# Kernel optimization log

Hardware: AMD Instinct MI355X
Metric: run time of the kernel (lower is better)

The kernel has to match this reference:

```python
import jax, jax.numpy as jnp
import numpy as np

N_NODES = 100000
N_EDGES = 1600000
D_IN = 128
D_OUT = 128


def setup_inputs() -> dict:
    key = jax.random.key(0)
    k1, k2, k3, k4, k5 = jax.random.split(key, 5)
    h = jax.random.normal(k1, (N_NODES, D_IN), dtype=jnp.float32)
    src = jax.random.randint(k2, (N_EDGES,), 0, N_NODES, dtype=jnp.int64)
    dst = jax.random.randint(k3, (N_EDGES,), 0, N_NODES, dtype=jnp.int64)
    # Glorot-ish init for linear weights (PyTorch nn.Linear style: [out, in])
    scale = 1.0 / np.sqrt(D_IN)
    W_self = jax.random.uniform(k4, (D_OUT, D_IN), jnp.float32, -scale, scale)
    W_neigh = jax.random.uniform(k5, (D_OUT, D_IN), jnp.float32, -scale, scale)
    b = jnp.zeros((D_OUT,), dtype=jnp.float32)
    return {"h": h, "src": src, "dst": dst, "W_self": W_self,
            "W_neigh": W_neigh, "b": b}


def reference(h, src, dst, W_self, W_neigh, b):
    n_nodes = h.shape[0]
    # neighbor gather + segment-mean over in-neighbors (DGL fn.copy_u + fn.mean)
    msg = h[src]                                            # [E, D_in]
    neigh_sum = jax.ops.segment_sum(msg, dst, num_segments=n_nodes)
    deg = jax.ops.segment_sum(jnp.ones_like(dst, dtype=h.dtype), dst,
                              num_segments=n_nodes)         # [N]
    h_neigh = neigh_sum / jnp.maximum(deg, 1.0)[:, None]    # mean; 0 for isolated
    # SAGEConv mean: fc_self(h) + fc_neigh(h_neigh) + bias
    out = h @ W_self.T + h_neigh @ W_neigh.T + b
    return out
```

## Files before the change

kernel.cpp:

```cpp
#include <hip/hip_runtime.h>
#include <stdint.h>

#define NN 100000
#define NE 1600000
#define DD 128
#define NTILES ((NN + 127) / 128)
#define NB 512
#define CHUNK (NE / NB)
#define NBUCK ((NN + 255) / 256)
#define BCAP 4608
#define QCAP 1536

typedef __bf16 bf16x8 __attribute__((ext_vector_type(8)));
typedef float f32x4 __attribute__((ext_vector_type(4)));
typedef float f32x2 __attribute__((ext_vector_type(2)));

__device__ __forceinline__ unsigned int f2bf2(float a, float b) {
  union { float f; unsigned u; } x, y;
  x.f = a; y.f = b;
  unsigned ua = x.u + (0x7FFFu + ((x.u >> 16) & 1u));
  unsigned ub = y.u + (0x7FFFu + ((y.u >> 16) & 1u));
  return (ua >> 16) | (ub & 0xFFFF0000u);
}

__global__ __launch_bounds__(256) void zero_kernel(int* __restrict__ gcur) {
  int t = blockIdx.x * 256 + threadIdx.x;
  if (t < NBUCK) gcur[t] = 0;
}

__global__ __launch_bounds__(256) void convert_scatter_kernel(
    const float4* __restrict__ hp, uint2* __restrict__ h8,
    uint4* __restrict__ hbf, const int* __restrict__ src,
    const int* __restrict__ dst, int* __restrict__ gcur,
    unsigned* __restrict__ ebuf) {
  __shared__ int lhp[512];
  __shared__ int lbase[NBUCK];
  __shared__ int lcur[NBUCK];
  __shared__ int gstart[NBUCK];
  __shared__ unsigned sdata[CHUNK];
  __shared__ int sgpos[CHUNK];
  int t = threadIdx.x, b = blockIdx.x;
  int gid = b * 256 + t;
  float4 a = hp[2 * gid], c = hp[2 * gid + 1];
  int lo = __builtin_amdgcn_cvt_pk_fp8_f32(a.x, a.y, 0, false);
  lo = __builtin_amdgcn_cvt_pk_fp8_f32(a.z, a.w, lo, true);
  int hi = __builtin_amdgcn_cvt_pk_fp8_f32(c.x, c.y, 0, false);
  hi = __builtin_amdgcn_cvt_pk_fp8_f32(c.z, c.w, hi, true);
  h8[gid] = make_uint2((unsigned)lo, (unsigned)hi);

  uint4 q;
  q.x = f2bf2(a.x, a.y);
  q.y = f2bf2(a.z, a.w);
  q.z = f2bf2(c.x, c.y);
  q.w = f2bf2(c.z, c.w);
  int m = t >> 4, c8 = t & 15;
  int rt = b & 7, kc = c8 >> 2, quad = c8 & 3;
  hbf[(size_t)(b >> 3) * 2048 + (((rt << 2) + kc) << 6) + (quad << 4) + m] = q;

  if (b >= NB) return;

  lhp[t] = 0;
  lhp[t + 256] = 0;
  __syncthreads();
  int e0 = b * CHUNK;
  for (int e = e0 + t; e < e0 + CHUNK; e += 256)
    atomicAdd(&lhp[dst[e] >> 8], 1);
  __syncthreads();
  int c0 = lhp[t], c1 = lhp[t + 256];
  for (int d = 1; d < 512; d <<= 1) {
    int x0 = (t >= d) ? lhp[t - d] : 0;
    int x1 = ((t + 256) >= d) ? lhp[t + 256 - d] : 0;
    __syncthreads();
    lhp[t] += x0;
    lhp[t + 256] += x1;
    __syncthreads();
  }
  if (t < NBUCK) {
    lbase[t] = lhp[t] - c0;
    lcur[t] = 0;
    gstart[t] = t * BCAP + (c0 ? atomicAdd(&gcur[t], c0) : 0);
  }
  int i2 = t + 256;
  if (i2 < NBUCK) {
    lbase[i2] = lhp[i2] - c1;
    lcur[i2] = 0;
    gstart[i2] = i2 * BCAP + (c1 ? atomicAdd(&gcur[i2], c1) : 0);
  }
  __syncthreads();
  for (int e = e0 + t; e < e0 + CHUNK; e += 256) {
    int d = dst[e], s = src[e];
    int bk = d >> 8;
    int slot = atomicAdd(&lcur[bk], 1);
    int lp = lbase[bk] + slot;
    sdata[lp] = ((unsigned)(d & 255) << 24) | (unsigned)s;
    sgpos[lp] = gstart[bk] + slot;
  }
  __syncthreads();
  for (int j = t; j < CHUNK; j += 256) ebuf[sgpos[j]] = sdata[j];
}

__device__ __forceinline__ void acc16p(f32x2* a, uint4 u) {
  a[0] += __builtin_amdgcn_cvt_pk_f32_fp8(u.x, false);
  a[1] += __builtin_amdgcn_cvt_pk_f32_fp8(u.x, true);
  a[2] += __builtin_amdgcn_cvt_pk_f32_fp8(u.y, false);
  a[3] += __builtin_amdgcn_cvt_pk_f32_fp8(u.y, true);
  a[4] += __builtin_amdgcn_cvt_pk_f32_fp8(u.z, false);
  a[5] += __builtin_amdgcn_cvt_pk_f32_fp8(u.z, true);
  a[6] += __builtin_amdgcn_cvt_pk_f32_fp8(u.w, false);
  a[7] += __builtin_amdgcn_cvt_pk_f32_fp8(u.w, true);
}

__global__ __launch_bounds__(256, 8) void gather_bucket_kernel(
    const unsigned* __restrict__ ebuf, const int* __restrict__ gcur,
    const uint4* __restrict__ h8, uint4* __restrict__ hfrag) {
  __shared__ int hist[64], st[64], cur[64];
  __shared__ int ssort[QCAP];
  int t = threadIdx.x, bid = blockIdx.x;
  int g = bid >> 2, qt = bid & 3;
  int base = g * BCAP;
  int cnt = gcur[g];
  int lo = qt * 64;
  if (t < 64) hist[t] = 0;
  __syncthreads();
  for (int j = t; j < cnt; j += 256) {
    int dn = (int)(ebuf[base + j] >> 24) - lo;
    if ((unsigned)dn < 64u) atomicAdd(&hist[dn], 1);
  }
  __syncthreads();
  if (t < 64) st[t] = hist[t];
  __syncthreads();
  for (int d = 1; d < 64; d <<= 1) {
    int x = (t < 64 && t >= d) ? st[t - d] : 0;
    __syncthreads();
    if (t < 64) st[t] += x;
    __syncthreads();
  }
  if (t < 64) {
    int s = st[t] - hist[t];
    st[t] = s;
    cur[t] = s;
  }
  __syncthreads();
  for (int j = t; j < cnt; j += 256) {
    unsigned e = ebuf[base + j];
    int dn = (int)(e >> 24) - lo;
    if ((unsigned)dn < 64u) {
      int pos = atomicAdd(&cur[dn], 1);
      if (pos < QCAP) ssort[pos] = (int)(e & 0x00FFFFFFu);
    }
  }
  __syncthreads();
  int grp = t >> 3, l = t & 7;
  uint4* bp = hfrag + (size_t)(bid >> 1) * 2048;
#pragma unroll 1
  for (int rnd = 0; rnd < 2; rnd++) {
    int li = rnd * 32 + grp;
    int deg = hist[li];
    int j0 = st[li];
    f32x2 a[8];
#pragma unroll
    for (int i = 0; i < 8; i++) a[i] = f32x2{0.f, 0.f};
    int jmax = deg & ~3;
    if (jmax > 0) {
      int s0 = ssort[j0], s1 = ssort[j0 + 1], s2 = ssort[j0 + 2], s3 = ssort[j0 + 3];
      uint4 u0 = h8[(size_t)s0 * 8 + l];
      uint4 u1 = h8[(size_t)s1 * 8 + l];
      uint4 u2 = h8[(size_t)s2 * 8 + l];
      uint4 u3 = h8[(size_t)s3 * 8 + l];
      for (int j4 = 4; j4 < jmax; j4 += 4) {
        int t0 = ssort[j0 + j4], t1 = ssort[j0 + j4 + 1];
        int t2 = ssort[j0 + j4 + 2], t3 = ssort[j0 + j4 + 3];
        uint4 v0 = h8[(size_t)t0 * 8 + l];
        uint4 v1 = h8[(size_t)t1 * 8 + l];
        uint4 v2 = h8[(size_t)t2 * 8 + l];
        uint4 v3 = h8[(size_t)t3 * 8 + l];
        acc16p(a, u0); acc16p(a, u1); acc16p(a, u2); acc16p(a, u3);
        u0 = v0; u1 = v1; u2 = v2; u3 = v3;
      }
      acc16p(a, u0); acc16p(a, u1); acc16p(a, u2); acc16p(a, u3);
    }
    for (int j2 = jmax; j2 < deg; j2++) acc16p(a, h8[(size_t)ssort[j0 + j2] * 8 + l]);
    float sc = (deg > 0) ? (1.0f / (float)deg) : 0.0f;
    f32x2 s2 = {sc, sc};
#pragma unroll
    for (int i = 0; i < 8; i++) a[i] *= s2;
    uint4 r0, r1;
    r0.x = f2bf2(a[0].x, a[0].y);  r0.y = f2bf2(a[1].x, a[1].y);
    r0.z = f2bf2(a[2].x, a[2].y);  r0.w = f2bf2(a[3].x, a[3].y);
    r1.x = f2bf2(a[4].x, a[4].y);  r1.y = f2bf2(a[5].x, a[5].y);
    r1.z = f2bf2(a[6].x, a[6].y);  r1.w = f2bf2(a[7].x, a[7].y);
    int r = ((qt & 1) << 6) + li;
    int rt = r >> 4, m = r & 15;
    int kc = l >> 1, quad = (l & 1) << 1;
    int slot = (((rt << 2) + kc) << 6) + (quad << 4) + m;
    bp[slot] = r0;
    bp[slot + 16] = r1;
  }
}

__device__ __forceinline__ void stage_w(const float* __restrict__ X,
                                        uint4* buf, int t) {
#pragma unroll
  for (int i = 0; i < 8; i++) {
    int id = t + (i << 8);
    int r = id >> 4;
    int c8 = id & 15;
    const float4* p = (const float4*)(X + (size_t)r * DD + (c8 << 3));
    float4 v0 = p[0], v1 = p[1];
    uint4 q;
    q.x = f2bf2(v0.x, v0.y);
    q.y = f2bf2(v0.z, v0.w);
    q.z = f2bf2(v1.x, v1.y);
    q.w = f2bf2(v1.z, v1.w);
    int rt = r >> 4, m = r & 15, kc = c8 >> 2, quad = c8 & 3;
    buf[(((rt << 2) + kc) << 6) + (quad << 4) + m] = q;
  }
}

__device__ __forceinline__ void compute_reg(const uint4* a, const uint4* sWb,
                                            f32x4 acc[2][8], int lane) {
#pragma unroll
  for (int kc = 0; kc < 4; kc++) {
    bf16x8 bfr[8];
#pragma unroll
    for (int n = 0; n < 8; n++)
      bfr[n] = *(const bf16x8*)&sWb[(((n << 2) + kc) << 6) + lane];
    bf16x8 a0 = *(const bf16x8*)&a[kc];
    bf16x8 a1 = *(const bf16x8*)&a[4 + kc];
#pragma unroll
    for (int n = 0; n < 8; n++) {
      acc[0][n] = __builtin_amdgcn_mfma_f32_16x16x32_bf16(a0, bfr[n], acc[0][n], 0, 0, 0);
      acc[1][n] = __builtin_amdgcn_mfma_f32_16x16x32_bf16(a1, bfr[n], acc[1][n], 0, 0, 0);
    }
  }
}

__global__ __launch_bounds__(256, 4) void gemm_kernel(
    const uint4* __restrict__ hbf, const uint4* __restrict__ hfrag,
    const float* __restrict__ Wself, const float* __restrict__ Wneigh,
    const float* __restrict__ bias, float* __restrict__ out) {
  __shared__ uint4 sW[2048];
  int t = threadIdx.x;
  int wv = t >> 6;
  int lane = t & 63;
  int row0 = blockIdx.x * 128;

  const uint4* fb1 = hbf + (size_t)blockIdx.x * 2048;
  const uint4* fb2 = hfrag + (size_t)blockIdx.x * 2048;
  uint4 a1[8], a2[8];
#pragma unroll
  for (int kc = 0; kc < 4; kc++) {
    int s0 = ((((wv * 2 + 0) << 2) + kc) << 6) + lane;
    int s1 = ((((wv * 2 + 1) << 2) + kc) << 6) + lane;
    a1[kc] = fb1[s0]; a1[4 + kc] = fb1[s1];
    a2[kc] = fb2[s0]; a2[4 + kc] = fb2[s1];
  }

  f32x4 acc[2][8];
#pragma unroll
  for (int i = 0; i < 2; i++)
#pragma unroll
    for (int n = 0; n < 8; n++) acc[i][n] = f32x4{0.f, 0.f, 0.f, 0.f};

  stage_w(Wself, sW, t);
  __syncthreads();
  compute_reg(a1, sW, acc, lane);
  __syncthreads();
  stage_w(Wneigh, sW, t);
  __syncthreads();
  compute_reg(a2, sW, acc, lane);

  int col = lane & 15, rq = lane >> 4;
  float bv[8];
#pragma unroll
  for (int n = 0; n < 8; n++) bv[n] = bias[n * 16 + col];
#pragma unroll
  for (int rt = 0; rt < 2; rt++) {
    int rb = row0 + (wv * 2 + rt) * 16 + rq * 4;
#pragma unroll
    for (int r = 0; r < 4; r++) {
      int row = rb + r;
      if (row < NN) {
        float* op = out + (size_t)row * DD + col;
#pragma unroll
        for (int n = 0; n < 8; n++) op[n * 16] = acc[rt][n][r] + bv[n];
      }
    }
  }
}

extern "C" void kernel_launch(void* const* d_in, const int* in_sizes, int n_in,
                              void* d_out, int out_size, void* d_ws, size_t ws_size,
                              hipStream_t stream) {
  const float* h      = (const float*)d_in[0];
  const int*   src    = (const int*)d_in[1];
  const int*   dst    = (const int*)d_in[2];
  const float* Wself  = (const float*)d_in[3];
  const float* Wneigh = (const float*)d_in[4];
  const float* bias   = (const float*)d_in[5];
  float* out = (float*)d_out;

  char* ws = (char*)d_ws;
  unsigned* h8       = (unsigned*)ws;
  unsigned* hbf      = (unsigned*)(ws + 12800000);
  unsigned* hfrag    = (unsigned*)(ws + 38424576);
  unsigned* ebuf     = (unsigned*)(ws + 64049152);
  int*      gcur     = (int*)(ws + 71256064);

  zero_kernel<<<2, 256, 0, stream>>>(gcur);
  convert_scatter_kernel<<<6250, 256, 0, stream>>>((const float4*)h, (uint2*)h8,
                                                   (uint4*)hbf, src, dst, gcur,
                                                   ebuf);
  gather_bucket_kernel<<<NBUCK * 4, 256, 0, stream>>>(ebuf, gcur,
                                                      (const uint4*)h8,
                                                      (uint4*)hfrag);
  gemm_kernel<<<NTILES, 256, 0, stream>>>((const uint4*)hbf, (const uint4*)hfrag,
                                          Wself, Wneigh, bias, out);
}
```

Baseline: 203.3 us.

## Split convert from scatter kernel and use eighth-bucket gather blocks

The fused convert+scatter kernel becomes two kernels: a 512-block coarse edge scatter and a separate 6250-block fp8/bf16 convert kernel, so the heavy shared-memory scatter blocks no longer share a launch with the lightweight convert blocks. The gather kernel now splits each 256-node bucket into 8 blocks of 32 destination nodes instead of 4 blocks of 64, each doing one round. This doubles gather block count for more parallelism and shorter per-block tails. The cost is that each gather block rescans the full bucket edge list, so those reads double, plus an extra kernel launch. The per-sub-bucket sort capacity also drops to 1024.

```diff
diff --git a/kernel.cpp b/kernel.cpp
--- a/kernel.cpp
+++ b/kernel.cpp
@@ -9,7 +9,7 @@
 #define CHUNK (NE / NB)
 #define NBUCK ((NN + 255) / 256)
 #define BCAP 4608
-#define QCAP 1536
+#define OCAP 1024
 
 typedef __bf16 bf16x8 __attribute__((ext_vector_type(8)));
 typedef float f32x4 __attribute__((ext_vector_type(4)));
@@ -28,17 +28,9 @@
   if (t < NBUCK) gcur[t] = 0;
 }
 
-__global__ __launch_bounds__(256) void convert_scatter_kernel(
+__global__ __launch_bounds__(256) void convert_kernel(
     const float4* __restrict__ hp, uint2* __restrict__ h8,
-    uint4* __restrict__ hbf, const int* __restrict__ src,
-    const int* __restrict__ dst, int* __restrict__ gcur,
-    unsigned* __restrict__ ebuf) {
-  __shared__ int lhp[512];
-  __shared__ int lbase[NBUCK];
-  __shared__ int lcur[NBUCK];
-  __shared__ int gstart[NBUCK];
-  __shared__ unsigned sdata[CHUNK];
-  __shared__ int sgpos[CHUNK];
+    uint4* __restrict__ hbf) {
   int t = threadIdx.x, b = blockIdx.x;
   int gid = b * 256 + t;
   float4 a = hp[2 * gid], c = hp[2 * gid + 1];
@@ -56,9 +48,18 @@
   int m = t >> 4, c8 = t & 15;
   int rt = b & 7, kc = c8 >> 2, quad = c8 & 3;
   hbf[(size_t)(b >> 3) * 2048 + (((rt << 2) + kc) << 6) + (quad << 4) + m] = q;
-
-  if (b >= NB) return;
-
+}
+
+__global__ __launch_bounds__(256) void coarse_scatter_kernel(
+    const int* __restrict__ src, const int* __restrict__ dst,
+    int* __restrict__ gcur, unsigned* __restrict__ ebuf) {
+  __shared__ int lhp[512];
+  __shared__ int lbase[NBUCK];
+  __shared__ int lcur[NBUCK];
+  __shared__ int gstart[NBUCK];
+  __shared__ unsigned sdata[CHUNK];
+  __shared__ int sgpos[CHUNK];
+  int t = threadIdx.x, b = blockIdx.x;
   lhp[t] = 0;
   lhp[t + 256] = 0;
   __syncthreads();
@@ -113,29 +114,29 @@
 __global__ __launch_bounds__(256, 8) void gather_bucket_kernel(
     const unsigned* __restrict__ ebuf, const int* __restrict__ gcur,
     const uint4* __restrict__ h8, uint4* __restrict__ hfrag) {
-  __shared__ int hist[64], st[64], cur[64];
-  __shared__ int ssort[QCAP];
+  __shared__ int hist[32], st[32], cur[32];
+  __shared__ int ssort[OCAP];
   int t = threadIdx.x, bid = blockIdx.x;
-  int g = bid >> 2, qt = bid & 3;
+  int g = bid >> 3, ot = bid & 7;
   int base = g * BCAP;
   int cnt = gcur[g];
-  int lo = qt * 64;
-  if (t < 64) hist[t] = 0;
+  int lo = ot * 32;
+  if (t < 32) hist[t] = 0;
   __syncthreads();
   for (int j = t; j < cnt; j += 256) {
     int dn = (int)(ebuf[base + j] >> 24) - lo;
-    if ((unsigned)dn < 64u) atomicAdd(&hist[dn], 1);
-  }
-  __syncthreads();
-  if (t < 64) st[t] = hist[t];
-  __syncthreads();
-  for (int d = 1; d < 64; d <<= 1) {
-    int x = (t < 64 && t >= d) ? st[t - d] : 0;
+    if ((unsigned)dn < 32u) atomicAdd(&hist[dn], 1);
+  }
+  __syncthreads();
+  if (t < 32) st[t] = hist[t];
+  __syncthreads();
+  for (int d = 1; d < 32; d <<= 1) {
+    int x = (t < 32 && t >= d) ? st[t - d] : 0;
     __syncthreads();
-    if (t < 64) st[t] += x;
+    if (t < 32) st[t] += x;
     __syncthreads();
   }
-  if (t < 64) {
+  if (t < 32) {
     int s = st[t] - hist[t];
     st[t] = s;
     cur[t] = s;
@@ -144,58 +145,55 @@
   for (int j = t; j < cnt; j += 256) {
     unsigned e = ebuf[base + j];
     int dn = (int)(e >> 24) - lo;
-    if ((unsigned)dn < 64u) {
+    if ((unsigned)dn < 32u) {
       int pos = atomicAdd(&cur[dn], 1);
-      if (pos < QCAP) ssort[pos] = (int)(e & 0x00FFFFFFu);
+      if (pos < OCAP) ssort[pos] = (int)(e & 0x00FFFFFFu);
     }
   }
   __syncthreads();
   int grp = t >> 3, l = t & 7;
-  uint4* bp = hfrag + (size_t)(bid >> 1) * 2048;
-#pragma unroll 1
-  for (int rnd = 0; rnd < 2; rnd++) {
-    int li = rnd * 32 + grp;
-    int deg = hist[li];
-    int j0 = st[li];
-    f32x2 a[8];
-#pragma unroll
-    for (int i = 0; i < 8; i++) a[i] = f32x2{0.f, 0.f};
-    int jmax = deg & ~3;
-    if (jmax > 0) {
-      int s0 = ssort[j0], s1 = ssort[j0 + 1], s2 = ssort[j0 + 2], s3 = ssort[j0 + 3];
-      uint4 u0 = h8[(size_t)s0 * 8 + l];
-      uint4 u1 = h8[(size_t)s1 * 8 + l];
-      uint4 u2 = h8[(size_t)s2 * 8 + l];
-      uint4 u3 = h8[(size_t)s3 * 8 + l];
-      for (int j4 = 4; j4 < jmax; j4 += 4) {
-        int t0 = ssort[j0 + j4], t1 = ssort[j0 + j4 + 1];
-        int t2 = ssort[j0 + j4 + 2], t3 = ssort[j0 + j4 + 3];
-        uint4 v0 = h8[(size_t)t0 * 8 + l];
-        uint4 v1 = h8[(size_t)t1 * 8 + l];
-        uint4 v2 = h8[(size_t)t2 * 8 + l];
-        uint4 v3 = h8[(size_t)t3 * 8 + l];
-        acc16p(a, u0); acc16p(a, u1); acc16p(a, u2); acc16p(a, u3);
-        u0 = v0; u1 = v1; u2 = v2; u3 = v3;
-      }
+  int tile = g * 2 + (ot >> 2);
+  uint4* bp = hfrag + (size_t)tile * 2048;
+  int deg = hist[grp];
+  int j0 = st[grp];
+  f32x2 a[8];
+#pragma unroll
+  for (int i = 0; i < 8; i++) a[i] = f32x2{0.f, 0.f};
+  int jmax = deg & ~3;
+  if (jmax > 0) {
+    int s0 = ssort[j0], s1 = ssort[j0 + 1], s2 = ssort[j0 + 2], s3 = ssort[j0 + 3];
+    uint4 u0 = h8[(size_t)s0 * 8 + l];
+    uint4 u1 = h8[(size_t)s1 * 8 + l];
+    uint4 u2 = h8[(size_t)s2 * 8 + l];
+    uint4 u3 = h8[(size_t)s3 * 8 + l];
+    for (int j4 = 4; j4 < jmax; j4 += 4) {
+      int t0 = ssort[j0 + j4], t1 = ssort[j0 + j4 + 1];
+      int t2 = ssort[j0 + j4 + 2], t3 = ssort[j0 + j4 + 3];
+      uint4 v0 = h8[(size_t)t0 * 8 + l];
+      uint4 v1 = h8[(size_t)t1 * 8 + l];
+      uint4 v2 = h8[(size_t)t2 * 8 + l];
+      uint4 v3 = h8[(size_t)t3 * 8 + l];
       acc16p(a, u0); acc16p(a, u1); acc16p(a, u2); acc16p(a, u3);
+      u0 = v0; u1 = v1; u2 = v2; u3 = v3;
     }
-    for (int j2 = jmax; j2 < deg; j2++) acc16p(a, h8[(size_t)ssort[j0 + j2] * 8 + l]);
-    float sc = (deg > 0) ? (1.0f / (float)deg) : 0.0f;
-    f32x2 s2 = {sc, sc};
-#pragma unroll
-    for (int i = 0; i < 8; i++) a[i] *= s2;
-    uint4 r0, r1;
-    r0.x = f2bf2(a[0].x, a[0].y);  r0.y = f2bf2(a[1].x, a[1].y);
-    r0.z = f2bf2(a[2].x, a[2].y);  r0.w = f2bf2(a[3].x, a[3].y);
-    r1.x = f2bf2(a[4].x, a[4].y);  r1.y = f2bf2(a[5].x, a[5].y);
-    r1.z = f2bf2(a[6].x, a[6].y);  r1.w = f2bf2(a[7].x, a[7].y);
-    int r = ((qt & 1) << 6) + li;
-    int rt = r >> 4, m = r & 15;
-    int kc = l >> 1, quad = (l & 1) << 1;
-    int slot = (((rt << 2) + kc) << 6) + (quad << 4) + m;
-    bp[slot] = r0;
-    bp[slot + 16] = r1;
-  }
+    acc16p(a, u0); acc16p(a, u1); acc16p(a, u2); acc16p(a, u3);
+  }
+  for (int j2 = jmax; j2 < deg; j2++) acc16p(a, h8[(size_t)ssort[j0 + j2] * 8 + l]);
+  float sc = (deg > 0) ? (1.0f / (float)deg) : 0.0f;
+  f32x2 s2 = {sc, sc};
+#pragma unroll
+  for (int i = 0; i < 8; i++) a[i] *= s2;
+  uint4 r0, r1;
+  r0.x = f2bf2(a[0].x, a[0].y);  r0.y = f2bf2(a[1].x, a[1].y);
+  r0.z = f2bf2(a[2].x, a[2].y);  r0.w = f2bf2(a[3].x, a[3].y);
+  r1.x = f2bf2(a[4].x, a[4].y);  r1.y = f2bf2(a[5].x, a[5].y);
+  r1.z = f2bf2(a[6].x, a[6].y);  r1.w = f2bf2(a[7].x, a[7].y);
+  int r = ((ot & 3) << 5) + grp;
+  int rt = r >> 4, m = r & 15;
+  int kc = l >> 1, quad = (l & 1) << 1;
+  int slot = (((rt << 2) + kc) << 6) + (quad << 4) + m;
+  bp[slot] = r0;
+  bp[slot + 16] = r1;
 }
 
 __device__ __forceinline__ void stage_w(const float* __restrict__ X,
@@ -308,10 +306,10 @@
   int*      gcur     = (int*)(ws + 71256064);
 
   zero_kernel<<<2, 256, 0, stream>>>(gcur);
-  convert_scatter_kernel<<<6250, 256, 0, stream>>>((const float4*)h, (uint2*)h8,
-                                                   (uint4*)hbf, src, dst, gcur,
-                                                   ebuf);
-  gather_bucket_kernel<<<NBUCK * 4, 256, 0, stream>>>(ebuf, gcur,
+  coarse_scatter_kernel<<<NB, 256, 0, stream>>>(src, dst, gcur, ebuf);
+  convert_kernel<<<6250, 256, 0, stream>>>((const float4*)h, (uint2*)h8,
+                                           (uint4*)hbf);
+  gather_bucket_kernel<<<NBUCK * 8, 256, 0, stream>>>(ebuf, gcur,
                                                       (const uint4*)h8,
                                                       (uint4*)hfrag);
   gemm_kernel<<<NTILES, 256, 0, stream>>>((const uint4*)hbf, (const uint4*)hfrag,
```

After: 220.7 us. 1.09x slower.
